# Kernel optimization log

Measured on AMD Instinct MI355X. Metric: run time of the kernel, lower is better.

Reference implementation:

```python
import jax, jax.numpy as jnp
import numpy as np
import math

B, L, D, H = 4, 2048, 512, 8
DH = D // H
FACTOR = 5.0
EPS = 1e-9
# static top-k count: min(L_q, max(1, int(factor * log(L_q + eps))))
K_TOP = min(L, max(1, int(FACTOR * math.log(L + EPS))))  # = 38
SCALE = 1.0 / math.sqrt(DH)


def setup_inputs() -> dict:
    key = jax.random.key(0)
    ks = jax.random.split(key, 9)
    s = 1.0 / math.sqrt(D)
    return {
        "x": jax.random.normal(ks[0], (B, L, D), jnp.float32),
        "Wq": jax.random.normal(ks[1], (D, D), jnp.float32) * s,
        "bq": jax.random.normal(ks[2], (D,), jnp.float32) * 0.01,
        "Wk": jax.random.normal(ks[3], (D, D), jnp.float32) * s,
        "bk": jax.random.normal(ks[4], (D,), jnp.float32) * 0.01,
        "Wv": jax.random.normal(ks[5], (D, D), jnp.float32) * s,
        "bv": jax.random.normal(ks[6], (D,), jnp.float32) * 0.01,
        "Wo": jax.random.normal(ks[7], (D, D), jnp.float32) * s,
        "bo": jax.random.normal(ks[8], (D,), jnp.float32) * 0.01,
    }


def _project(x, W, b):
    # [B, L, D] -> [B*H, L, DH]
    y = x @ W + b
    return y.reshape(B, L, H, DH).transpose(0, 2, 1, 3).reshape(B * H, L, DH)


def reference(x, Wq, bq, Wk, bk, Wv, bv, Wo, bo):
    Q = _project(x, Wq, bq)
    K = _project(x, Wk, bk)
    V = _project(x, Wv, bv)

    # full scores for sparsity measure: [BH, L, L]
    scores = jnp.einsum('bqd,bkd->bqk', Q, K) * SCALE
    M = scores.max(axis=-1) - scores.mean(axis=-1)  # [BH, L]
    _, top_idx = jax.lax.top_k(M, K_TOP)            # [BH, K_TOP]

    # gather sparse queries, sparse attention
    Q_sparse = jnp.take_along_axis(Q, top_idx[:, :, None], axis=1)  # [BH, K_TOP, DH]
    scores_sparse = jnp.einsum('bqd,bkd->bqk', Q_sparse, K) * SCALE
    attn = jax.nn.softmax(scores_sparse, axis=-1)
    context_sparse = attn @ V                                        # [BH, K_TOP, DH]

    # mean-filled context, scatter sparse results back
    V_mean = V.mean(axis=1, keepdims=True)                           # [BH, 1, DH]
    context = jnp.broadcast_to(V_mean, (B * H, L, DH))
    bidx = jnp.arange(B * H)[:, None]
    context = context.at[bidx, top_idx, :].set(context_sparse)

    # merge heads, output projection
    out = context.reshape(B, H, L, DH).transpose(0, 2, 1, 3).reshape(B, L, D)
    return out @ Wo + bo
```

## Files before the change

### kernel.cpp

```cpp
#include <hip/hip_runtime.h>

#define BB   4
#define LL   2048
#define DD   512
#define HH   8
#define DH   64
#define BH   32
#define KTOP 38
#define NCAND 64
#define SCALEF 0.125f

#define NSP  16
#define CHK  128
#define QPAD 48
#define SCS  132
#define VST  66

typedef __attribute__((ext_vector_type(8))) short bf16x8;
typedef __attribute__((ext_vector_type(8))) unsigned short ushort8;
typedef __attribute__((ext_vector_type(4))) float f32x4;

__device__ __forceinline__ ushort f32_to_bf16_rn(float x) {
    unsigned u = __float_as_uint(x);
    u += 0x7fffu + ((u >> 16) & 1u);
    return (ushort)(u >> 16);
}
__device__ __forceinline__ float bf16_to_f32(ushort h) {
    return __uint_as_float(((unsigned)h) << 16);
}
__device__ __forceinline__ unsigned int pack_hl(float x) {
    ushort h = f32_to_bf16_rn(x);
    ushort l = f32_to_bf16_rn(x - bf16_to_f32(h));
    return ((unsigned int)l << 16) | (unsigned int)h;
}

__global__ __launch_bounds__(256) void split_x(const float* __restrict__ X,
                                               ushort* __restrict__ XH,
                                               ushort* __restrict__ XL) {
    const size_t c = (size_t)blockIdx.x * 256 + threadIdx.x;
    const float4 v = *(const float4*)&X[c * 4];
    ushort4 h, l;
    h.x = f32_to_bf16_rn(v.x); l.x = f32_to_bf16_rn(v.x - bf16_to_f32(h.x));
    h.y = f32_to_bf16_rn(v.y); l.y = f32_to_bf16_rn(v.y - bf16_to_f32(h.y));
    h.z = f32_to_bf16_rn(v.z); l.z = f32_to_bf16_rn(v.z - bf16_to_f32(h.z));
    h.w = f32_to_bf16_rn(v.w); l.w = f32_to_bf16_rn(v.w - bf16_to_f32(h.w));
    *(ushort4*)&XH[c * 4] = h;
    *(ushort4*)&XL[c * 4] = l;
}

__global__ __launch_bounds__(256) void split_wT(const float* __restrict__ W0,
                                                const float* __restrict__ W1,
                                                const float* __restrict__ W2,
                                                const float* __restrict__ W3,
                                                ushort* __restrict__ WTH,
                                                ushort* __restrict__ WTL) {
    __shared__ float tile[32][33];
    const int z = blockIdx.z;
    const float* W = (z == 0) ? W0 : (z == 1) ? W1 : (z == 2) ? W2 : W3;
    ushort* oh = WTH + (size_t)z * DD * DD;
    ushort* ol = WTL + (size_t)z * DD * DD;
    const int n0 = blockIdx.x * 32, k0 = blockIdx.y * 32;
    const int t = threadIdx.x;
    const int r = t >> 5, c = t & 31;
    #pragma unroll
    for (int i = 0; i < 4; i++)
        tile[r + i * 8][c] = W[(size_t)(k0 + r + i * 8) * DD + n0 + c];
    __syncthreads();
    #pragma unroll
    for (int i = 0; i < 4; i++) {
        int row = r + i * 8;
        float v = tile[c][row];
        ushort h = f32_to_bf16_rn(v);
        oh[(size_t)(n0 + row) * DD + k0 + c] = h;
        ol[(size_t)(n0 + row) * DD + k0 + c] = f32_to_bf16_rn(v - bf16_to_f32(h));
    }
}

template <int APERM, int YPERM, int WSPLIT>
__global__ __launch_bounds__(256) void mfma_gemm(const ushort* __restrict__ AH,
                                                 const ushort* __restrict__ AL,
                                                 const ushort* __restrict__ BTH,
                                                 const ushort* __restrict__ BTL,
                                                 const float* __restrict__ bias,
                                                 float* __restrict__ Y,
                                                 ushort* __restrict__ YH) {
    __shared__ ushort BHs[64 * 40];
    __shared__ ushort BLs[64 * 40];

    const int t = threadIdx.x;
    const int w = t >> 6, lane = t & 63;
    const int quad = lane >> 4, n16 = lane & 15;
    const int row0 = blockIdx.y * 128;
    const int n0   = blockIdx.x * 64;

    f32x4 acc[2][4] = {};

    size_t arow_off[2];
    #pragma unroll
    for (int mt = 0; mt < 2; mt++) {
        int R = row0 + w * 32 + mt * 16 + n16;
        if (APERM) {
            int b = R >> 11, l = R & 2047;
            arow_off[mt] = ((size_t)b * HH) * LL * DH + (size_t)l * DH;
        } else {
            arow_off[mt] = (size_t)R * DD;
        }
    }

    const int brow = t >> 2, bc8 = t & 3;

    for (int k0 = 0; k0 < DD; k0 += 32) {
        {
            const size_t goff = (size_t)(n0 + brow) * DD + k0 + bc8 * 8;
            const uint4 vh = *(const uint4*)&BTH[goff];
            const uint4 vl = *(const uint4*)&BTL[goff];
            *(uint4*)&BHs[brow * 40 + bc8 * 8] = vh;
            *(uint4*)&BLs[brow * 40 + bc8 * 8] = vl;
        }
        bf16x8 ah[2], al[2];
        #pragma unroll
        for (int mt = 0; mt < 2; mt++) {
            int k = k0 + quad * 8;
            size_t off;
            if (APERM) {
                int h = k >> 6, dh = k & 63;
                off = arow_off[mt] + (size_t)h * LL * DH + dh;
            } else {
                off = arow_off[mt] + k;
            }
            ah[mt] = *(const bf16x8*)&AH[off];
            al[mt] = *(const bf16x8*)&AL[off];
        }
        __syncthreads();

        bf16x8 bh[4], bl[4];
        #pragma unroll
        for (int nt = 0; nt < 4; nt++) {
            int off = (nt * 16 + n16) * 40 + quad * 8;
            bh[nt] = *(const bf16x8*)&BHs[off];
            bl[nt] = *(const bf16x8*)&BLs[off];
        }
        #pragma unroll
        for (int mt = 0; mt < 2; mt++)
            #pragma unroll
            for (int nt = 0; nt < 4; nt++) {
                acc[mt][nt] = __builtin_amdgcn_mfma_f32_16x16x32_bf16(ah[mt], bh[nt], acc[mt][nt], 0, 0, 0);
                acc[mt][nt] = __builtin_amdgcn_mfma_f32_16x16x32_bf16(ah[mt], bl[nt], acc[mt][nt], 0, 0, 0);
                acc[mt][nt] = __builtin_amdgcn_mfma_f32_16x16x32_bf16(al[mt], bh[nt], acc[mt][nt], 0, 0, 0);
            }
        __syncthreads();
    }

    #pragma unroll
    for (int mt = 0; mt < 2; mt++)
        #pragma unroll
        for (int nt = 0; nt < 4; nt++) {
            const int c = n0 + nt * 16 + n16;
            const float bv = bias[c];
            #pragma unroll
            for (int r = 0; r < 4; r++) {
                int m = w * 32 + mt * 16 + quad * 4 + r;
                int R = row0 + m;
                float v = acc[mt][nt][r] + bv;
                size_t off;
                if (YPERM) {
                    int b = R >> 11, l = R & 2047;
                    int h = c >> 6, dh = c & 63;
                    off = (((size_t)(b * HH + h)) * LL + l) * DH + dh;
                } else {
                    off = (size_t)R * DD + c;
                }
                Y[off] = v;
                if (WSPLIT) YH[off] = f32_to_bf16_rn(v);
            }
        }
}

__global__ __launch_bounds__(256) void mean_partial(const float* __restrict__ Kp,
                                                    const float* __restrict__ Vp,
                                                    float* __restrict__ partial) {
    __shared__ float red[256];
    const int bh = blockIdx.x;
    const int srcI = blockIdx.y;
    const int z  = blockIdx.z;
    const float* src = srcI ? Vp : Kp;
    const int t = threadIdx.x;
    const int d = t & 63, ch = t >> 6;
    const int l0 = z * 128 + ch * 32;
    float s = 0.f;
    for (int l = l0; l < l0 + 32; l++)
        s += src[((size_t)bh * LL + l) * DH + d];
    red[t] = s;
    __syncthreads();
    if (t < 64)
        partial[((size_t)((bh * 2 + srcI) * 16 + z)) * 64 + t] =
            red[t] + red[t + 64] + red[t + 128] + red[t + 192];
}

__global__ __launch_bounds__(64) void mean_reduce(const float* __restrict__ partial,
                                                  float* __restrict__ Kmean,
                                                  float* __restrict__ Vmean) {
    const int bh = blockIdx.x;
    const int srcI = blockIdx.y;
    const int t  = threadIdx.x;
    float s = 0.f;
    #pragma unroll
    for (int z = 0; z < 16; z++)
        s += partial[((size_t)((bh * 2 + srcI) * 16 + z)) * 64 + t];
    float* dst = srcI ? Vmean : Kmean;
    dst[bh * DH + t] = s * (1.0f / LL);
}

__global__ __launch_bounds__(256) void mfma_stats(const float* __restrict__ Qp,
                                                  const ushort* __restrict__ KH,
                                                  const float* __restrict__ Kmean,
                                                  float* __restrict__ M) {
    __shared__ ushort KS[128 * 72];
    __shared__ float  Km[64];
    __shared__ float  mdS[128];

    const int bh = blockIdx.y;
    const int q0 = blockIdx.x * 128;
    const int t    = threadIdx.x;
    const int w    = t >> 6;
    const int lane = t & 63;
    const int quad = lane >> 4;
    const int n16  = lane & 15;

    if (t < 64) Km[t] = Kmean[bh * DH + t];
    __syncthreads();
    if (t < 128) {
        const float4* qr = (const float4*)&Qp[((size_t)bh * LL + q0 + t) * DH];
        const float4* km4 = (const float4*)Km;
        float md = 0.f;
        #pragma unroll
        for (int i = 0; i < 16; i++) {
            float4 a = qr[i], b = km4[i];
            md += a.x * b.x + a.y * b.y + a.z * b.z + a.w * b.w;
        }
        mdS[t] = md;
    }

    bf16x8 aH[2][2], aL[2][2];
    #pragma unroll
    for (int mt = 0; mt < 2; mt++) {
        const float* qrp = &Qp[((size_t)bh * LL + q0 + w * 32 + mt * 16 + n16) * DH + quad * 8];
        float v[16];
        *(float4*)&v[0]  = *(const float4*)(qrp);
        *(float4*)&v[4]  = *(const float4*)(qrp + 4);
        *(float4*)&v[8]  = *(const float4*)(qrp + 32);
        *(float4*)&v[12] = *(const float4*)(qrp + 36);
        #pragma unroll
        for (int j = 0; j < 8; j++) {
            ushort h0 = f32_to_bf16_rn(v[j]);
            aH[mt][0][j] = (short)h0;
            aL[mt][0][j] = (short)f32_to_bf16_rn(v[j] - bf16_to_f32(h0));
            ushort h1 = f32_to_bf16_rn(v[8 + j]);
            aH[mt][1][j] = (short)h1;
            aL[mt][1][j] = (short)f32_to_bf16_rn(v[8 + j] - bf16_to_f32(h1));
        }
    }

    f32x4 maxv[2] = {{-3.4e38f, -3.4e38f, -3.4e38f, -3.4e38f},
                     {-3.4e38f, -3.4e38f, -3.4e38f, -3.4e38f}};

    for (int kt0 = 0; kt0 < LL; kt0 += 128) {
        __syncthreads();
        #pragma unroll
        for (int i = 0; i < 4; i++) {
            int f = i * 256 + t;
            int row = f >> 3, c8 = f & 7;
            const uint4 v = *(const uint4*)&KH[((size_t)(bh * LL + kt0 + row)) * DH + c8 * 8];
            *(uint4*)&KS[row * 72 + c8 * 8] = v;
        }
        __syncthreads();

        for (int ktl = 0; ktl < 128; ktl += 16) {
            const ushort* bp = &KS[(size_t)(ktl + n16) * 72 + quad * 8];
            bf16x8 bH0 = *(const bf16x8*)(bp);
            bf16x8 bH1 = *(const bf16x8*)(bp + 32);
            #pragma unroll
            for (int mt = 0; mt < 2; mt++) {
                f32x4 acc = {0.f, 0.f, 0.f, 0.f};
                acc = __builtin_amdgcn_mfma_f32_16x16x32_bf16(aH[mt][0], bH0, acc, 0, 0, 0);
                acc = __builtin_amdgcn_mfma_f32_16x16x32_bf16(aH[mt][1], bH1, acc, 0, 0, 0);
                acc = __builtin_amdgcn_mfma_f32_16x16x32_bf16(aL[mt][0], bH0, acc, 0, 0, 0);
                acc = __builtin_amdgcn_mfma_f32_16x16x32_bf16(aL[mt][1], bH1, acc, 0, 0, 0);
                maxv[mt][0] = fmaxf(maxv[mt][0], acc[0]);
                maxv[mt][1] = fmaxf(maxv[mt][1], acc[1]);
                maxv[mt][2] = fmaxf(maxv[mt][2], acc[2]);
                maxv[mt][3] = fmaxf(maxv[mt][3], acc[3]);
            }
        }
    }

    #pragma unroll
    for (int off = 1; off < 16; off <<= 1)
        #pragma unroll
        for (int mt = 0; mt < 2; mt++)
            #pragma unroll
            for (int r = 0; r < 4; r++)
                maxv[mt][r] = fmaxf(maxv[mt][r], __shfl_xor(maxv[mt][r], off));

    if (n16 == 0) {
        #pragma unroll
        for (int mt = 0; mt < 2; mt++)
            #pragma unroll
            for (int r = 0; r < 4; r++) {
                int lq = w * 32 + mt * 16 + quad * 4 + r;
                M[(size_t)bh * LL + q0 + lq] = SCALEF * maxv[mt][r] - SCALEF * mdS[lq];
            }
    }
}

__global__ __launch_bounds__(256) void topk_radix(const float* __restrict__ M,
                                                  int* __restrict__ out_idx) {
    __shared__ unsigned hist[4096];
    __shared__ unsigned segc[256];
    __shared__ unsigned suf[256];
    __shared__ int sb1, sc1, sb2;
    __shared__ int ncnt;
    const int bh = blockIdx.x;
    const int t  = threadIdx.x;

    unsigned key[8];
    #pragma unroll
    for (int i = 0; i < 8; i++) {
        unsigned u = __float_as_uint(M[(size_t)bh * LL + i * 256 + t]);
        key[i] = (u & 0x80000000u) ? ~u : (u | 0x80000000u);
    }

    #pragma unroll
    for (int i = 0; i < 16; i++) hist[t * 16 + i] = 0;
    if (t == 0) ncnt = 0;
    __syncthreads();
    #pragma unroll
    for (int i = 0; i < 8; i++) atomicAdd(&hist[key[i] >> 20], 1u);
    __syncthreads();
    unsigned s = 0;
    #pragma unroll
    for (int i = 0; i < 16; i++) s += hist[t * 16 + i];
    segc[t] = s;
    __syncthreads();
    if (t == 0) {
        unsigned run = 0;
        for (int i = 255; i >= 0; i--) { suf[i] = run; run += segc[i]; }
    }
    __syncthreads();
    if (suf[t] < NCAND && suf[t] + segc[t] >= NCAND) {
        unsigned c = suf[t];
        for (int j = 15; j >= 0; j--) {
            int b = t * 16 + j;
            if (c + hist[b] >= NCAND) { sb1 = b; sc1 = (int)c; break; }
            c += hist[b];
        }
    }
    __syncthreads();
    const unsigned b1 = (unsigned)sb1;
    const int c1 = sc1;

    #pragma unroll
    for (int i = 0; i < 16; i++) hist[t * 16 + i] = 0;
    __syncthreads();
    #pragma unroll
    for (int i = 0; i < 8; i++)
        if ((key[i] >> 20) == b1) atomicAdd(&hist[(key[i] >> 8) & 0xfffu], 1u);
    __syncthreads();
    s = 0;
    #pragma unroll
    for (int i = 0; i < 16; i++) s += hist[t * 16 + i];
    segc[t] = s;
    __syncthreads();
    if (t == 0) {
        unsigned run = 0;
        for (int i = 255; i >= 0; i--) { suf[i] = run; run += segc[i]; }
    }
    __syncthreads();
    const int need2 = NCAND - c1;
    if ((int)suf[t] < need2 && (int)(suf[t] + segc[t]) >= need2) {
        unsigned c = suf[t];
        for (int j = 15; j >= 0; j--) {
            int b = t * 16 + j;
            if ((int)(c + hist[b]) >= need2) { sb2 = b; break; }
            c += hist[b];
        }
    }
    __syncthreads();
    const unsigned b2 = (unsigned)sb2;

    #pragma unroll
    for (int i = 0; i < 8; i++)
        if ((key[i] >> 20) > b1) {
            int p = atomicAdd(&ncnt, 1);
            out_idx[bh * NCAND + p] = i * 256 + t;
        }
    __syncthreads();
    #pragma unroll
    for (int i = 0; i < 8; i++)
        if ((key[i] >> 20) == b1 && ((key[i] >> 8) & 0xfffu) > b2) {
            int p = atomicAdd(&ncnt, 1);
            out_idx[bh * NCAND + p] = i * 256 + t;
        }
    __syncthreads();
    #pragma unroll
    for (int i = 0; i < 8; i++)
        if ((key[i] >> 20) == b1 && ((key[i] >> 8) & 0xfffu) == b2) {
            int p = atomicAdd(&ncnt, 1);
            if (p < NCAND) out_idx[bh * NCAND + p] = i * 256 + t;
        }
}

__global__ __launch_bounds__(256) void exact_partial(const float* __restrict__ Qp,
                                                     const float* __restrict__ Kp,
                                                     const int* __restrict__ CAND,
                                                     float* __restrict__ EMP) {
    __shared__ float Qs[64][65];
    __shared__ float Ks[64][65];
    __shared__ int   cidx[64];
    const int bh = blockIdx.y;
    const int chunk = blockIdx.x;
    const int t = threadIdx.x;
    const int tx = t & 15, ty = t >> 4;

    if (t < 64) cidx[t] = CAND[bh * NCAND + t];
    __syncthreads();
    #pragma unroll
    for (int i = 0; i < 4; i++) {
        int f = i * 256 + t;
        int row = f >> 4, c4 = f & 15;
        const float4 v = *(const float4*)&Qp[((size_t)bh * LL + cidx[row]) * DH + c4 * 4];
        *(float4*)&Qs[row][c4 * 4] = v;
    }

    float mx[4] = {-3.4e38f, -3.4e38f, -3.4e38f, -3.4e38f};

    for (int kt = 0; kt < 4; kt++) {
        __syncthreads();
        #pragma unroll
        for (int i = 0; i < 4; i++) {
            int f = i * 256 + t;
            int row = f >> 4, c4 = f & 15;
            const float4 v = *(const float4*)&Kp[((size_t)(bh * LL + chunk * 256 + kt * 64 + row)) * DH + c4 * 4];
            *(float4*)&Ks[row][c4 * 4] = v;
        }
        __syncthreads();
        float acc[4][4] = {};
        #pragma unroll 8
        for (int dd = 0; dd < 64; dd++) {
            float a[4], b[4];
            #pragma unroll
            for (int i = 0; i < 4; i++) a[i] = Qs[ty * 4 + i][dd];
            #pragma unroll
            for (int j = 0; j < 4; j++) b[j] = Ks[tx * 4 + j][dd];
            #pragma unroll
            for (int i = 0; i < 4; i++)
                #pragma unroll
                for (int j = 0; j < 4; j++) acc[i][j] += a[i] * b[j];
        }
        #pragma unroll
        for (int i = 0; i < 4; i++)
            #pragma unroll
            for (int j = 0; j < 4; j++) mx[i] = fmaxf(mx[i], acc[i][j]);
    }

    #pragma unroll
    for (int off = 1; off < 16; off <<= 1)
        #pragma unroll
        for (int i = 0; i < 4; i++)
            mx[i] = fmaxf(mx[i], __shfl_xor(mx[i], off));

    if (tx == 0) {
        #pragma unroll
        for (int i = 0; i < 4; i++)
            EMP[((size_t)bh * NCAND + ty * 4 + i) * 8 + chunk] = mx[i];
    }
}

__global__ __launch_bounds__(64) void select_kernel(const float* __restrict__ EMP,
                                                    const int* __restrict__ CAND,
                                                    const float* __restrict__ Qp,
                                                    const float* __restrict__ Kmean,
                                                    int* __restrict__ TIDX) {
    __shared__ float Km[64];
    const int bh = blockIdx.x;
    const int t  = threadIdx.x;
    Km[t] = Kmean[bh * DH + t];
    __syncthreads();

    const int qi = CAND[bh * NCAND + t];
    float mx = -3.4e38f;
    #pragma unroll
    for (int c = 0; c < 8; c++) mx = fmaxf(mx, EMP[((size_t)bh * NCAND + t) * 8 + c]);

    const float4* qr = (const float4*)&Qp[((size_t)bh * LL + qi) * DH];
    const float4* km4 = (const float4*)Km;
    float md = 0.f;
    #pragma unroll
    for (int i = 0; i < 16; i++) {
        float4 a = qr[i], b = km4[i];
        md += a.x * b.x + a.y * b.y + a.z * b.z + a.w * b.w;
    }
    float v = SCALEF * mx - SCALEF * md;

    for (int it = 0; it < KTOP; it++) {
        float bv = v; int bq = qi;
        #pragma unroll
        for (int off = 1; off < 64; off <<= 1) {
            float ov = __shfl_xor(bv, off);
            int   oq = __shfl_xor(bq, off);
            if (ov > bv || (ov == bv && oq < bq)) { bv = ov; bq = oq; }
        }
        if (t == 0) TIDX[bh * KTOP + it] = bq;
        if (qi == bq) v = -3.4e38f;
    }
}

__global__ __launch_bounds__(256) void fill_kernel(const float* __restrict__ Vmean,
                                                   ushort* __restrict__ CH,
                                                   ushort* __restrict__ CL) {
    const size_t c = (size_t)blockIdx.x * 256 + threadIdx.x;
    const int d4 = (int)(c & 15) * 4;
    const int bh = (int)(c >> 15);
    const float4 v = *(const float4*)&Vmean[bh * DH + d4];
    ushort4 h, l;
    h.x = f32_to_bf16_rn(v.x); l.x = f32_to_bf16_rn(v.x - bf16_to_f32(h.x));
    h.y = f32_to_bf16_rn(v.y); l.y = f32_to_bf16_rn(v.y - bf16_to_f32(h.y));
    h.z = f32_to_bf16_rn(v.z); l.z = f32_to_bf16_rn(v.z - bf16_to_f32(h.z));
    h.w = f32_to_bf16_rn(v.w); l.w = f32_to_bf16_rn(v.w - bf16_to_f32(h.w));
    *(ushort4*)&CH[c * 4] = h;
    *(ushort4*)&CL[c * 4] = l;
}

__global__ __launch_bounds__(256) void sparse_partial(const float* __restrict__ Qp,
                                                      const ushort* __restrict__ KH,
                                                      const float* __restrict__ Vp,
                                                      const int* __restrict__ TIDX,
                                                      float* __restrict__ OPART,
                                                      float* __restrict__ MPART,
                                                      float* __restrict__ LPART) {
    __shared__ float sc[QPAD * SCS];
    __shared__ unsigned int Vhl[CHK * VST];
    const int bh = blockIdx.y;
    const int ck = blockIdx.x;
    const int k0 = ck * CHK;
    const int t = threadIdx.x;
    const int w = t >> 6, lane = t & 63;
    const int quad = lane >> 4, n16 = lane & 15;
    const int mt = w;

    #pragma unroll
    for (int i = 0; i < 8; i++) {
        int e = i * 256 + t;
        int key = e >> 4, c4 = e & 15;
        const float4 v = *(const float4*)&Vp[((size_t)(bh * LL + k0 + key)) * DH + c4 * 4];
        uint4 p;
        p.x = pack_hl(v.x); p.y = pack_hl(v.y);
        p.z = pack_hl(v.z); p.w = pack_hl(v.w);
        *(uint4*)&Vhl[key * VST + c4 * 4] = p;
    }

    if (mt < 3) {
        bf16x8 aH[2], aL[2];
        {
            int q = mt * 16 + n16;
            int qq = q < KTOP ? q : (KTOP - 1);
            const float* qp = &Qp[((size_t)bh * LL + TIDX[bh * KTOP + qq]) * DH];
            #pragma unroll
            for (int kf = 0; kf < 2; kf++) {
                float v[8];
                *(float4*)&v[0] = *(const float4*)(qp + kf * 32 + quad * 8);
                *(float4*)&v[4] = *(const float4*)(qp + kf * 32 + quad * 8 + 4);
                #pragma unroll
                for (int j = 0; j < 8; j++) {
                    ushort h = f32_to_bf16_rn(v[j]);
                    aH[kf][j] = (short)h;
                    aL[kf][j] = (short)f32_to_bf16_rn(v[j] - bf16_to_f32(h));
                }
            }
        }
        #pragma unroll
        for (int nt = 0; nt < 8; nt++) {
            f32x4 acc = {0.f, 0.f, 0.f, 0.f};
            #pragma unroll
            for (int kf = 0; kf < 2; kf++) {
                bf16x8 b = *(const bf16x8*)&KH[((size_t)(bh * LL + k0 + nt * 16 + n16)) * DH + kf * 32 + quad * 8];
                acc = __builtin_amdgcn_mfma_f32_16x16x32_bf16(aH[kf], b, acc, 0, 0, 0);
                acc = __builtin_amdgcn_mfma_f32_16x16x32_bf16(aL[kf], b, acc, 0, 0, 0);
            }
            #pragma unroll
            for (int r = 0; r < 4; r++)
                sc[(mt * 16 + quad * 4 + r) * SCS + nt * 16 + n16] = acc[r];
        }
    }
    __syncthreads();

    for (int row = w; row < KTOP; row += 4) {
        float v0 = sc[row * SCS + lane];
        float v1 = sc[row * SCS + 64 + lane];
        float m = fmaxf(v0, v1);
        #pragma unroll
        for (int off = 1; off < 64; off <<= 1)
            m = fmaxf(m, __shfl_xor(m, off));
        const float ms = m * SCALEF;
        float e0 = __expf(v0 * SCALEF - ms);
        float e1 = __expf(v1 * SCALEF - ms);
        float l = e0 + e1;
        #pragma unroll
        for (int off = 1; off < 64; off <<= 1)
            l += __shfl_xor(l, off);
        sc[row * SCS + lane]      = e0;
        sc[row * SCS + 64 + lane] = e1;
        if (lane == 0) {
            MPART[((size_t)ck * BH + bh) * KTOP + row] = ms;
            LPART[((size_t)ck * BH + bh) * KTOP + row] = l;
        }
    }
    __syncthreads();

    if (mt < 3) {
        f32x4 acc[4] = {};
        #pragma unroll
        for (int kf = 0; kf < 4; kf++) {
            bf16x8 ph, pl;
            {
                const float* pp = &sc[(mt * 16 + n16) * SCS + kf * 32 + quad * 8];
                float v[8];
                *(float4*)&v[0] = *(const float4*)(pp);
                *(float4*)&v[4] = *(const float4*)(pp + 4);
                #pragma unroll
                for (int j = 0; j < 8; j++) {
                    ushort h = f32_to_bf16_rn(v[j]);
                    ph[j] = (short)h;
                    pl[j] = (short)f32_to_bf16_rn(v[j] - bf16_to_f32(h));
                }
            }
            #pragma unroll
            for (int nt = 0; nt < 4; nt++) {
                unsigned int u[8];
                #pragma unroll
                for (int j = 0; j < 8; j++)
                    u[j] = Vhl[(kf * 32 + quad * 8 + j) * VST + nt * 16 + n16];
                bf16x8 vh, vl;
                #pragma unroll
                for (int j = 0; j < 8; j++) {
                    vh[j] = (short)(u[j] & 0xffffu);
                    vl[j] = (short)(u[j] >> 16);
                }
                acc[nt] = __builtin_amdgcn_mfma_f32_16x16x32_bf16(ph, vh, acc[nt], 0, 0, 0);
                acc[nt] = __builtin_amdgcn_mfma_f32_16x16x32_bf16(ph, vl, acc[nt], 0, 0, 0);
                acc[nt] = __builtin_amdgcn_mfma_f32_16x16x32_bf16(pl, vh, acc[nt], 0, 0, 0);
            }
        }
        #pragma unroll
        for (int nt = 0; nt < 4; nt++)
            #pragma unroll
            for (int r = 0; r < 4; r++) {
                int q = mt * 16 + quad * 4 + r;
                if (q < KTOP)
                    OPART[(((size_t)ck * BH + bh) * KTOP + q) * DH + nt * 16 + n16] = acc[nt][r];
            }
    }
}

__global__ __launch_bounds__(256) void sparse_combine(const float* __restrict__ OPART,
                                                      const float* __restrict__ MPART,
                                                      const float* __restrict__ LPART,
                                                      const int* __restrict__ TIDX,
                                                      ushort* __restrict__ CH,
                                                      ushort* __restrict__ CL) {
    __shared__ float wts[NSP][KTOP];
    __shared__ float inv[KTOP];
    __shared__ int   tq[KTOP];
    const int bh = blockIdx.x;
    const int t  = threadIdx.x;
    if (t < KTOP) {
        float m[NSP];
        float mx = -3.4e38f;
        #pragma unroll
        for (int c = 0; c < NSP; c++) {
            m[c] = MPART[((size_t)c * BH + bh) * KTOP + t];
            mx = fmaxf(mx, m[c]);
        }
        float L = 0.f;
        #pragma unroll
        for (int c = 0; c < NSP; c++) {
            float wc = __expf(m[c] - mx);
            wts[c][t] = wc;
            L += wc * LPART[((size_t)c * BH + bh) * KTOP + t];
        }
        inv[t] = 1.0f / L;
        tq[t] = TIDX[bh * KTOP + t];
    }
    __syncthreads();
    for (int i = 0; i < 10; i++) {
        int idx = i * 256 + t;
        if (idx >= KTOP * DH) break;
        int q = idx >> 6, d = idx & 63;
        float o = 0.f;
        #pragma unroll
        for (int c = 0; c < NSP; c++)
            o += wts[c][q] * OPART[(((size_t)c * BH + bh) * KTOP + q) * DH + d];
        float val = o * inv[q];
        size_t off = ((size_t)bh * LL + tq[q]) * DH + d;
        ushort h = f32_to_bf16_rn(val);
        CH[off] = h;
        CL[off] = f32_to_bf16_rn(val - bf16_to_f32(h));
    }
}

extern "C" void kernel_launch(void* const* d_in, const int* in_sizes, int n_in,
                              void* d_out, int out_size, void* d_ws, size_t ws_size,
                              hipStream_t stream) {
    const float* x  = (const float*)d_in[0];
    const float* Wq = (const float*)d_in[1];
    const float* bq = (const float*)d_in[2];
    const float* Wk = (const float*)d_in[3];
    const float* bk = (const float*)d_in[4];
    const float* Wv = (const float*)d_in[5];
    const float* bv = (const float*)d_in[6];
    const float* Wo = (const float*)d_in[7];
    const float* bo = (const float*)d_in[8];
    float* out = (float*)d_out;

    float* ws = (float*)d_ws;
    const size_t QSZ = (size_t)BH * LL * DH;
    float* Qp    = ws;
    float* Kp    = ws + QSZ;
    float* Vp    = ws + 2 * QSZ;
    float* Mp    = ws + 3 * QSZ;
    float* KMEAN = Mp + (size_t)BH * LL;
    float* VMEAN = KMEAN + BH * DH;
    int*   CAND  = (int*)(VMEAN + BH * DH);
    int*   TIDX  = CAND + BH * NCAND;
    float* EMP   = (float*)(TIDX + BH * KTOP);
    float* MEANP = EMP + (size_t)BH * NCAND * 8;
    ushort* WTH  = (ushort*)(ws + 3 * QSZ + 262144);
    ushort* WTL  = WTH + (size_t)4 * DD * DD;
    ushort* XH   = WTL + (size_t)4 * DD * DD;
    ushort* XL   = XH + QSZ;
    ushort* CH   = XH;
    ushort* CL   = XL;
    ushort* KH   = XL + QSZ;
    float* OPART = (float*)(KH + QSZ);
    float* MPART = OPART + (size_t)NSP * BH * KTOP * DH;
    float* LPART = MPART + (size_t)NSP * BH * KTOP;
    const size_t WOFF = (size_t)DD * DD;

    split_wT<<<dim3(16, 16, 4), 256, 0, stream>>>(Wq, Wk, Wv, Wo, WTH, WTL);
    split_x<<<(int)(QSZ / 1024), 256, 0, stream>>>(x, XH, XL);

    const dim3 gemm_grid(DD / 64, (BB * LL) / 128);
    mfma_gemm<0, 1, 0><<<gemm_grid, 256, 0, stream>>>(XH, XL, WTH,            WTL,            bq, Qp, nullptr);
    mfma_gemm<0, 1, 1><<<gemm_grid, 256, 0, stream>>>(XH, XL, WTH + WOFF,     WTL + WOFF,     bk, Kp, KH);
    mfma_gemm<0, 1, 0><<<gemm_grid, 256, 0, stream>>>(XH, XL, WTH + 2 * WOFF, WTL + 2 * WOFF, bv, Vp, nullptr);

    mean_partial<<<dim3(BH, 2, 16), 256, 0, stream>>>(Kp, Vp, MEANP);
    mean_reduce<<<dim3(BH, 2), 64, 0, stream>>>(MEANP, KMEAN, VMEAN);

    mfma_stats<<<dim3(LL / 128, BH), 256, 0, stream>>>(Qp, KH, KMEAN, Mp);

    topk_radix<<<BH, 256, 0, stream>>>(Mp, CAND);

    exact_partial<<<dim3(8, BH), 256, 0, stream>>>(Qp, Kp, CAND, EMP);

    select_kernel<<<BH, 64, 0, stream>>>(EMP, CAND, Qp, KMEAN, TIDX);

    fill_kernel<<<(int)(QSZ / 1024), 256, 0, stream>>>(VMEAN, CH, CL);

    sparse_partial<<<dim3(NSP, BH), 256, 0, stream>>>(Qp, KH, Vp, TIDX, OPART, MPART, LPART);
    sparse_combine<<<BH, 256, 0, stream>>>(OPART, MPART, LPART, TIDX, CH, CL);

    mfma_gemm<1, 0, 0><<<gemm_grid, 256, 0, stream>>>(CH, CL, WTH + 3 * WOFF, WTL + 3 * WOFF, bo, out, nullptr);
}
```

Before: 335.4 us.

## Fuse QKV projections into one launch and split stats kernel over key halves

The three Q/K/V projection GEMMs are merged into a single launch with a 24-wide column grid, where each block picks its weight slice, bias and output from its column index. The sparsity-stats kernel is split along the key dimension into two halves via a z grid dimension, so it launches twice as many blocks. Each half writes a partial max, and the top-k kernel combines them with the separately stored scaled mean-dot term. This cuts launch overhead and raises occupancy for the stats pass, at the cost of extra workspace and an extra read in top-k.

```diff
diff --git a/kernel.cpp b/kernel.cpp
--- a/kernel.cpp
+++ b/kernel.cpp
@@ -76,14 +76,17 @@
     }
 }
 
-template <int APERM, int YPERM, int WSPLIT>
-__global__ __launch_bounds__(256) void mfma_gemm(const ushort* __restrict__ AH,
-                                                 const ushort* __restrict__ AL,
-                                                 const ushort* __restrict__ BTH,
-                                                 const ushort* __restrict__ BTL,
-                                                 const float* __restrict__ bias,
-                                                 float* __restrict__ Y,
-                                                 ushort* __restrict__ YH) {
+__global__ __launch_bounds__(256) void mfma_gemm_qkv(const ushort* __restrict__ AH,
+                                                     const ushort* __restrict__ AL,
+                                                     const ushort* __restrict__ BTH,
+                                                     const ushort* __restrict__ BTL,
+                                                     const float* __restrict__ bq,
+                                                     const float* __restrict__ bk,
+                                                     const float* __restrict__ bv,
+                                                     float* __restrict__ Qp,
+                                                     float* __restrict__ Kp,
+                                                     float* __restrict__ Vp,
+                                                     ushort* __restrict__ KH) {
     __shared__ ushort BHs[64 * 40];
     __shared__ ushort BLs[64 * 40];
 
@@ -92,6 +95,90 @@
     const int quad = lane >> 4, n16 = lane & 15;
     const int row0 = blockIdx.y * 128;
     const int n0   = blockIdx.x * 64;
+    const int z    = n0 >> 9;
+    const int nloc0 = n0 & 511;
+
+    const float* bias = (z == 0) ? bq : (z == 1) ? bk : bv;
+    float* Y          = (z == 0) ? Qp : (z == 1) ? Kp : Vp;
+
+    f32x4 acc[2][4] = {};
+
+    size_t arow_off[2];
+    #pragma unroll
+    for (int mt = 0; mt < 2; mt++)
+        arow_off[mt] = (size_t)(row0 + w * 32 + mt * 16 + n16) * DD;
+
+    const int brow = t >> 2, bc8 = t & 3;
+    const size_t bbase = (size_t)z * DD * DD;
+
+    for (int k0 = 0; k0 < DD; k0 += 32) {
+        {
+            const size_t goff = bbase + (size_t)(nloc0 + brow) * DD + k0 + bc8 * 8;
+            const uint4 vh = *(const uint4*)&BTH[goff];
+            const uint4 vl = *(const uint4*)&BTL[goff];
+            *(uint4*)&BHs[brow * 40 + bc8 * 8] = vh;
+            *(uint4*)&BLs[brow * 40 + bc8 * 8] = vl;
+        }
+        bf16x8 ah[2], al[2];
+        #pragma unroll
+        for (int mt = 0; mt < 2; mt++) {
+            size_t off = arow_off[mt] + k0 + quad * 8;
+            ah[mt] = *(const bf16x8*)&AH[off];
+            al[mt] = *(const bf16x8*)&AL[off];
+        }
+        __syncthreads();
+
+        bf16x8 bh[4], bl[4];
+        #pragma unroll
+        for (int nt = 0; nt < 4; nt++) {
+            int off = (nt * 16 + n16) * 40 + quad * 8;
+            bh[nt] = *(const bf16x8*)&BHs[off];
+            bl[nt] = *(const bf16x8*)&BLs[off];
+        }
+        #pragma unroll
+        for (int mt = 0; mt < 2; mt++)
+            #pragma unroll
+            for (int nt = 0; nt < 4; nt++) {
+                acc[mt][nt] = __builtin_amdgcn_mfma_f32_16x16x32_bf16(ah[mt], bh[nt], acc[mt][nt], 0, 0, 0);
+                acc[mt][nt] = __builtin_amdgcn_mfma_f32_16x16x32_bf16(ah[mt], bl[nt], acc[mt][nt], 0, 0, 0);
+                acc[mt][nt] = __builtin_amdgcn_mfma_f32_16x16x32_bf16(al[mt], bh[nt], acc[mt][nt], 0, 0, 0);
+            }
+        __syncthreads();
+    }
+
+    #pragma unroll
+    for (int mt = 0; mt < 2; mt++)
+        #pragma unroll
+        for (int nt = 0; nt < 4; nt++) {
+            const int c = nloc0 + nt * 16 + n16;
+            const float bvv = bias[c];
+            const int h = c >> 6, dh = c & 63;
+            #pragma unroll
+            for (int r = 0; r < 4; r++) {
+                int R = row0 + w * 32 + mt * 16 + quad * 4 + r;
+                int b = R >> 11, l = R & 2047;
+                float v = acc[mt][nt][r] + bvv;
+                size_t off = (((size_t)(b * HH + h)) * LL + l) * DH + dh;
+                Y[off] = v;
+                if (z == 1) KH[off] = f32_to_bf16_rn(v);
+            }
+        }
+}
+
+__global__ __launch_bounds__(256) void mfma_gemm_out(const ushort* __restrict__ AH,
+                                                     const ushort* __restrict__ AL,
+                                                     const ushort* __restrict__ BTH,
+                                                     const ushort* __restrict__ BTL,
+                                                     const float* __restrict__ bias,
+                                                     float* __restrict__ Y) {
+    __shared__ ushort BHs[64 * 40];
+    __shared__ ushort BLs[64 * 40];
+
+    const int t = threadIdx.x;
+    const int w = t >> 6, lane = t & 63;
+    const int quad = lane >> 4, n16 = lane & 15;
+    const int row0 = blockIdx.y * 128;
+    const int n0   = blockIdx.x * 64;
 
     f32x4 acc[2][4] = {};
 
@@ -99,12 +186,8 @@
     #pragma unroll
     for (int mt = 0; mt < 2; mt++) {
         int R = row0 + w * 32 + mt * 16 + n16;
-        if (APERM) {
-            int b = R >> 11, l = R & 2047;
-            arow_off[mt] = ((size_t)b * HH) * LL * DH + (size_t)l * DH;
-        } else {
-            arow_off[mt] = (size_t)R * DD;
-        }
+        int b = R >> 11, l = R & 2047;
+        arow_off[mt] = ((size_t)b * HH) * LL * DH + (size_t)l * DH;
     }
 
     const int brow = t >> 2, bc8 = t & 3;
@@ -121,13 +204,8 @@
         #pragma unroll
         for (int mt = 0; mt < 2; mt++) {
             int k = k0 + quad * 8;
-            size_t off;
-            if (APERM) {
-                int h = k >> 6, dh = k & 63;
-                off = arow_off[mt] + (size_t)h * LL * DH + dh;
-            } else {
-                off = arow_off[mt] + k;
-            }
+            int h = k >> 6, dh = k & 63;
+            size_t off = arow_off[mt] + (size_t)h * LL * DH + dh;
             ah[mt] = *(const bf16x8*)&AH[off];
             al[mt] = *(const bf16x8*)&AL[off];
         }
@@ -156,22 +234,11 @@
         #pragma unroll
         for (int nt = 0; nt < 4; nt++) {
             const int c = n0 + nt * 16 + n16;
-            const float bv = bias[c];
+            const float bvv = bias[c];
             #pragma unroll
             for (int r = 0; r < 4; r++) {
-                int m = w * 32 + mt * 16 + quad * 4 + r;
-                int R = row0 + m;
-                float v = acc[mt][nt][r] + bv;
-                size_t off;
-                if (YPERM) {
-                    int b = R >> 11, l = R & 2047;
-                    int h = c >> 6, dh = c & 63;
-                    off = (((size_t)(b * HH + h)) * LL + l) * DH + dh;
-                } else {
-                    off = (size_t)R * DD + c;
-                }
-                Y[off] = v;
-                if (WSPLIT) YH[off] = f32_to_bf16_rn(v);
+                int R = row0 + w * 32 + mt * 16 + quad * 4 + r;
+                Y[(size_t)R * DD + c] = acc[mt][nt][r] + bvv;
             }
         }
 }
@@ -214,31 +281,34 @@
 __global__ __launch_bounds__(256) void mfma_stats(const float* __restrict__ Qp,
                                                   const ushort* __restrict__ KH,
                                                   const float* __restrict__ Kmean,
-                                                  float* __restrict__ M) {
+                                                  float* __restrict__ MP,
+                                                  float* __restrict__ MMD) {
     __shared__ ushort KS[128 * 72];
     __shared__ float  Km[64];
-    __shared__ float  mdS[128];
 
     const int bh = blockIdx.y;
     const int q0 = blockIdx.x * 128;
+    const int z  = blockIdx.z;
     const int t    = threadIdx.x;
     const int w    = t >> 6;
     const int lane = t & 63;
     const int quad = lane >> 4;
     const int n16  = lane & 15;
 
-    if (t < 64) Km[t] = Kmean[bh * DH + t];
-    __syncthreads();
-    if (t < 128) {
-        const float4* qr = (const float4*)&Qp[((size_t)bh * LL + q0 + t) * DH];
-        const float4* km4 = (const float4*)Km;
-        float md = 0.f;
-        #pragma unroll
-        for (int i = 0; i < 16; i++) {
-            float4 a = qr[i], b = km4[i];
-            md += a.x * b.x + a.y * b.y + a.z * b.z + a.w * b.w;
-        }
-        mdS[t] = md;
+    if (z == 0) {
+        if (t < 64) Km[t] = Kmean[bh * DH + t];
+        __syncthreads();
+        if (t < 128) {
+            const float4* qr = (const float4*)&Qp[((size_t)bh * LL + q0 + t) * DH];
+            const float4* km4 = (const float4*)Km;
+            float md = 0.f;
+            #pragma unroll
+            for (int i = 0; i < 16; i++) {
+                float4 a = qr[i], b = km4[i];
+                md += a.x * b.x + a.y * b.y + a.z * b.z + a.w * b.w;
+            }
+            MMD[(size_t)bh * LL + q0 + t] = SCALEF * md;
+        }
     }
 
     bf16x8 aH[2][2], aL[2][2];
@@ -264,7 +334,8 @@
     f32x4 maxv[2] = {{-3.4e38f, -3.4e38f, -3.4e38f, -3.4e38f},
                      {-3.4e38f, -3.4e38f, -3.4e38f, -3.4e38f}};
 
-    for (int kt0 = 0; kt0 < LL; kt0 += 128) {
+    const int kbase = z * (LL / 2);
+    for (int kt0 = kbase; kt0 < kbase + LL / 2; kt0 += 128) {
         __syncthreads();
         #pragma unroll
         for (int i = 0; i < 4; i++) {
@@ -308,12 +379,13 @@
             #pragma unroll
             for (int r = 0; r < 4; r++) {
                 int lq = w * 32 + mt * 16 + quad * 4 + r;
-                M[(size_t)bh * LL + q0 + lq] = SCALEF * maxv[mt][r] - SCALEF * mdS[lq];
-            }
-    }
-}
-
-__global__ __launch_bounds__(256) void topk_radix(const float* __restrict__ M,
+                MP[((size_t)z * BH + bh) * LL + q0 + lq] = SCALEF * maxv[mt][r];
+            }
+    }
+}
+
+__global__ __launch_bounds__(256) void topk_radix(const float* __restrict__ MP,
+                                                  const float* __restrict__ MMD,
                                                   int* __restrict__ out_idx) {
     __shared__ unsigned hist[4096];
     __shared__ unsigned segc[256];
@@ -326,7 +398,10 @@
     unsigned key[8];
     #pragma unroll
     for (int i = 0; i < 8; i++) {
-        unsigned u = __float_as_uint(M[(size_t)bh * LL + i * 256 + t]);
+        size_t q = (size_t)i * 256 + t;
+        float v = fmaxf(MP[(size_t)bh * LL + q], MP[((size_t)BH + bh) * LL + q])
+                  - MMD[(size_t)bh * LL + q];
+        unsigned u = __float_as_uint(v);
         key[i] = (u & 0x80000000u) ? ~u : (u | 0x80000000u);
     }
 
@@ -727,14 +802,15 @@
     float* Qp    = ws;
     float* Kp    = ws + QSZ;
     float* Vp    = ws + 2 * QSZ;
-    float* Mp    = ws + 3 * QSZ;
-    float* KMEAN = Mp + (size_t)BH * LL;
+    float* MMD   = ws + 3 * QSZ;
+    float* KMEAN = MMD + (size_t)BH * LL;
     float* VMEAN = KMEAN + BH * DH;
     int*   CAND  = (int*)(VMEAN + BH * DH);
     int*   TIDX  = CAND + BH * NCAND;
     float* EMP   = (float*)(TIDX + BH * KTOP);
     float* MEANP = EMP + (size_t)BH * NCAND * 8;
-    ushort* WTH  = (ushort*)(ws + 3 * QSZ + 262144);
+    float* MP    = MEANP + 65536;
+    ushort* WTH  = (ushort*)(ws + 3 * QSZ + 524288);
     ushort* WTL  = WTH + (size_t)4 * DD * DD;
     ushort* XH   = WTL + (size_t)4 * DD * DD;
     ushort* XL   = XH + QSZ;
@@ -749,17 +825,15 @@
     split_wT<<<dim3(16, 16, 4), 256, 0, stream>>>(Wq, Wk, Wv, Wo, WTH, WTL);
     split_x<<<(int)(QSZ / 1024), 256, 0, stream>>>(x, XH, XL);
 
-    const dim3 gemm_grid(DD / 64, (BB * LL) / 128);
-    mfma_gemm<0, 1, 0><<<gemm_grid, 256, 0, stream>>>(XH, XL, WTH,            WTL,            bq, Qp, nullptr);
-    mfma_gemm<0, 1, 1><<<gemm_grid, 256, 0, stream>>>(XH, XL, WTH + WOFF,     WTL + WOFF,     bk, Kp, KH);
-    mfma_gemm<0, 1, 0><<<gemm_grid, 256, 0, stream>>>(XH, XL, WTH + 2 * WOFF, WTL + 2 * WOFF, bv, Vp, nullptr);
+    mfma_gemm_qkv<<<dim3(24, 64), 256, 0, stream>>>(XH, XL, WTH, WTL,
+                                                    bq, bk, bv, Qp, Kp, Vp, KH);
 
     mean_partial<<<dim3(BH, 2, 16), 256, 0, stream>>>(Kp, Vp, MEANP);
     mean_reduce<<<dim3(BH, 2), 64, 0, stream>>>(MEANP, KMEAN, VMEAN);
 
-    mfma_stats<<<dim3(LL / 128, BH), 256, 0, stream>>>(Qp, KH, KMEAN, Mp);
-
-    topk_radix<<<BH, 256, 0, stream>>>(Mp, CAND);
+    mfma_stats<<<dim3(16, BH, 2), 256, 0, stream>>>(Qp, KH, KMEAN, MP, MMD);
+
+    topk_radix<<<BH, 256, 0, stream>>>(MP, MMD, CAND);
 
     exact_partial<<<dim3(8, BH), 256, 0, stream>>>(Qp, Kp, CAND, EMP);
 
@@ -770,5 +844,5 @@
     sparse_partial<<<dim3(NSP, BH), 256, 0, stream>>>(Qp, KH, Vp, TIDX, OPART, MPART, LPART);
     sparse_combine<<<BH, 256, 0, stream>>>(OPART, MPART, LPART, TIDX, CH, CL);
 
-    mfma_gemm<1, 0, 0><<<gemm_grid, 256, 0, stream>>>(CH, CL, WTH + 3 * WOFF, WTL + 3 * WOFF, bo, out, nullptr);
-}
+    mfma_gemm_out<<<dim3(8, 64), 256, 0, stream>>>(CH, CL, WTH + 3 * WOFF, WTL + 3 * WOFF, bo, out);
+}
```

Measured after the change: 301.5 us. -10.1%, faster.
